# Kernel optimization log

Hardware: AMD Instinct MI355X
Metric: run time of the kernel (lower is better)

## Reference

```python
import jax, jax.numpy as jnp
import numpy as np

N, IN_CAPS, OUT_CH = 4096, 1152, 32
EPS = 1e-8

def squash(s, axis):
    # standard capsule squash: ||s||^2/(1+||s||^2) * s/||s||
    n2 = jnp.sum(s * s, axis=axis, keepdims=True)
    return (n2 / (1.0 + n2)) * s / jnp.sqrt(n2 + EPS)

def setup_inputs() -> dict:
    key = jax.random.key(0)
    k1, _ = jax.random.split(key)
    u_hat = jax.random.normal(k1, (N, IN_CAPS, OUT_CH), dtype=jnp.float32)
    # uniform routing prior: softmax of zeros over out_channels axis
    c = jnp.full((1, IN_CAPS, OUT_CH), 1.0 / OUT_CH, dtype=jnp.float32)
    return {"u_hat": u_hat, "c": c, "routings": 3}

def reference(u_hat, c, routings):
    out_channels = u_hat.shape[2]
    u = u_hat  # retain_grad=True: no stop_gradient on u
    for _ in range(routings - 1):
        v = squash(jnp.sum(u * c, axis=1), axis=1)          # (N, out_channels)
        b = u * v[:, None, :]                                # (N, in_caps, out_channels)
        c = jax.nn.softmax(b, axis=2)
    v = squash(jnp.sum(u_hat * c, axis=1), axis=1)
    return v[:, None, :] / 2.0 + 0.5                         # (N, 1, out_channels)
```

## Files before the change

kernel.cpp:

```cpp
#include <hip/hip_runtime.h>

#define IN_CAPS 1152
#define OUT_CH 32
#define PAD 33
#define BLOCK 576
#define NWAVES (BLOCK / 64)
#define ROWS_PER_THREAD (IN_CAPS / BLOCK)
#define F4_PER_THREAD (IN_CAPS * OUT_CH / 4 / BLOCK)
#define EPS 1e-8f

__global__ __launch_bounds__(BLOCK, 3)
void caps_route(const float* __restrict__ u_hat,
                const float* __restrict__ c0,
                const int* __restrict__ routings_p,
                float* __restrict__ out)
{
    __shared__ float u_s[IN_CAPS * PAD];
    __shared__ float swred[NWAVES * OUT_CH];
    __shared__ float vsh[OUT_CH];

    const int t = threadIdx.x;
    const int n = blockIdx.x;
    const int lane = t & 63;
    const int wave = t >> 6;

    const float4* __restrict__ u4 =
        reinterpret_cast<const float4*>(u_hat) + (size_t)n * (IN_CAPS * OUT_CH / 4);
    const float4* __restrict__ c4 = reinterpret_cast<const float4*>(c0);

    float p0 = 0.f, p1 = 0.f, p2 = 0.f, p3 = 0.f;
    #pragma unroll
    for (int k = 0; k < F4_PER_THREAD; ++k) {
        int f = t + k * BLOCK;
        float4 a = u4[f];
        float4 w = c4[f];
        int i  = f >> 3;
        int j0 = (f & 7) << 2;
        float* dst = &u_s[i * PAD + j0];
        dst[0] = a.x; dst[1] = a.y; dst[2] = a.z; dst[3] = a.w;
        p0 = fmaf(a.x, w.x, p0);
        p1 = fmaf(a.y, w.y, p1);
        p2 = fmaf(a.z, w.z, p2);
        p3 = fmaf(a.w, w.w, p3);
    }
    #pragma unroll
    for (int m = 8; m <= 32; m <<= 1) {
        p0 += __shfl_xor(p0, m);
        p1 += __shfl_xor(p1, m);
        p2 += __shfl_xor(p2, m);
        p3 += __shfl_xor(p3, m);
    }
    if (lane < 8) {
        swred[wave * OUT_CH + lane * 4 + 0] = p0;
        swred[wave * OUT_CH + lane * 4 + 1] = p1;
        swred[wave * OUT_CH + lane * 4 + 2] = p2;
        swred[wave * OUT_CH + lane * 4 + 3] = p3;
    }
    __syncthreads();
    if (t < OUT_CH) {
        float s = 0.f;
        #pragma unroll
        for (int w = 0; w < NWAVES; ++w) s += swred[w * OUT_CH + t];
        float n2 = s * s;
        #pragma unroll
        for (int m = 1; m <= 16; m <<= 1) n2 += __shfl_xor(n2, m);
        float scale = n2 / ((1.0f + n2) * sqrtf(n2 + EPS));
        vsh[t] = s * scale;
    }
    __syncthreads();

    const int iters = routings_p[0] - 1;
    for (int it = 0; it < iters; ++it) {
        float v[OUT_CH];
        #pragma unroll
        for (int j = 0; j < OUT_CH; ++j) v[j] = vsh[j];

        float acc[OUT_CH];
        #pragma unroll
        for (int j = 0; j < OUT_CH; ++j) acc[j] = 0.f;

        #pragma unroll
        for (int s = 0; s < ROWS_PER_THREAD; ++s) {
            const int i = t + s * BLOCK;
            const float* row = &u_s[i * PAD];
            float rr[OUT_CH], e[OUT_CH];
            float sum = 0.f;
            #pragma unroll
            for (int j = 0; j < OUT_CH; ++j) {
                rr[j] = row[j];
                e[j] = __expf(rr[j] * v[j]);
                sum += e[j];
            }
            float w = __builtin_amdgcn_rcpf(sum);
            #pragma unroll
            for (int j = 0; j < OUT_CH; ++j)
                acc[j] = fmaf(rr[j], e[j] * w, acc[j]);
        }

        #pragma unroll
        for (int j = 0; j < OUT_CH; ++j) {
            #pragma unroll
            for (int m = 1; m <= 32; m <<= 1)
                acc[j] += __shfl_xor(acc[j], m);
        }
        if (lane == 0) {
            #pragma unroll
            for (int j = 0; j < OUT_CH; ++j) swred[wave * OUT_CH + j] = acc[j];
        }
        __syncthreads();
        if (t < OUT_CH) {
            float s = 0.f;
            #pragma unroll
            for (int w = 0; w < NWAVES; ++w) s += swred[w * OUT_CH + t];
            float n2 = s * s;
            #pragma unroll
            for (int m = 1; m <= 16; m <<= 1) n2 += __shfl_xor(n2, m);
            float scale = n2 / ((1.0f + n2) * sqrtf(n2 + EPS));
            vsh[t] = s * scale;
        }
        __syncthreads();
    }

    if (t < OUT_CH) {
        out[(size_t)n * OUT_CH + t] = vsh[t] * 0.5f + 0.5f;
    }
}

extern "C" void kernel_launch(void* const* d_in, const int* in_sizes, int n_in,
                              void* d_out, int out_size, void* d_ws, size_t ws_size,
                              hipStream_t stream) {
    const float* u_hat   = (const float*)d_in[0];
    const float* c0      = (const float*)d_in[1];
    const int*   routing = (const int*)d_in[2];
    float* out = (float*)d_out;

    const int N = in_sizes[0] / (IN_CAPS * OUT_CH);
    caps_route<<<dim3(N), dim3(BLOCK), 0, stream>>>(u_hat, c0, routing, out);
}
```

Before: 971.6 us.

## Drop LDS staging of u_hat, re-read rows from global, use transpose-reduce

Removes the 147KB shared-memory copy of each sample's u_hat and instead re-reads rows from global memory (served by L2/MALL) in every routing iteration, with the block shrunk to 192 threads so more blocks fit per CU. The per-wave 32-channel shuffle reduction is replaced by a butterfly transpose-reduce that halves the live values at each stage, so the shuffle count drops from about 32x6 to about 32. The risk is extra global/L2 traffic, since each 147KB sample is read three times instead of once, in exchange for higher occupancy and no LDS capacity limit.

```diff
diff --git a/kernel.cpp b/kernel.cpp
--- a/kernel.cpp
+++ b/kernel.cpp
@@ -2,25 +2,23 @@
 
 #define IN_CAPS 1152
 #define OUT_CH 32
-#define PAD 33
-#define BLOCK 576
+#define BLOCK 192
 #define NWAVES (BLOCK / 64)
 #define ROWS_PER_THREAD (IN_CAPS / BLOCK)
 #define F4_PER_THREAD (IN_CAPS * OUT_CH / 4 / BLOCK)
 #define EPS 1e-8f
 
-__global__ __launch_bounds__(BLOCK, 3)
+__global__ __launch_bounds__(BLOCK, 4)
 void caps_route(const float* __restrict__ u_hat,
                 const float* __restrict__ c0,
                 const int* __restrict__ routings_p,
                 float* __restrict__ out)
 {
-    __shared__ float u_s[IN_CAPS * PAD];
     __shared__ float swred[NWAVES * OUT_CH];
     __shared__ float vsh[OUT_CH];
 
-    const int t = threadIdx.x;
-    const int n = blockIdx.x;
+    const int t    = threadIdx.x;
+    const int n    = blockIdx.x;
     const int lane = t & 63;
     const int wave = t >> 6;
 
@@ -31,13 +29,9 @@
     float p0 = 0.f, p1 = 0.f, p2 = 0.f, p3 = 0.f;
     #pragma unroll
     for (int k = 0; k < F4_PER_THREAD; ++k) {
-        int f = t + k * BLOCK;
-        float4 a = u4[f];
-        float4 w = c4[f];
-        int i  = f >> 3;
-        int j0 = (f & 7) << 2;
-        float* dst = &u_s[i * PAD + j0];
-        dst[0] = a.x; dst[1] = a.y; dst[2] = a.z; dst[3] = a.w;
+        const int f = t + k * BLOCK;
+        const float4 a = u4[f];
+        const float4 w = c4[f];
         p0 = fmaf(a.x, w.x, p0);
         p1 = fmaf(a.y, w.y, p1);
         p2 = fmaf(a.z, w.z, p2);
@@ -51,10 +45,8 @@
         p3 += __shfl_xor(p3, m);
     }
     if (lane < 8) {
-        swred[wave * OUT_CH + lane * 4 + 0] = p0;
-        swred[wave * OUT_CH + lane * 4 + 1] = p1;
-        swred[wave * OUT_CH + lane * 4 + 2] = p2;
-        swred[wave * OUT_CH + lane * 4 + 3] = p3;
+        float* dst = &swred[wave * OUT_CH + lane * 4];
+        dst[0] = p0; dst[1] = p1; dst[2] = p2; dst[3] = p3;
     }
     __syncthreads();
     if (t < OUT_CH) {
@@ -64,7 +56,7 @@
         float n2 = s * s;
         #pragma unroll
         for (int m = 1; m <= 16; m <<= 1) n2 += __shfl_xor(n2, m);
-        float scale = n2 / ((1.0f + n2) * sqrtf(n2 + EPS));
+        const float scale = n2 / ((1.0f + n2) * sqrtf(n2 + EPS));
         vsh[t] = s * scale;
     }
     __syncthreads();
@@ -82,31 +74,47 @@
         #pragma unroll
         for (int s = 0; s < ROWS_PER_THREAD; ++s) {
             const int i = t + s * BLOCK;
-            const float* row = &u_s[i * PAD];
-            float rr[OUT_CH], e[OUT_CH];
-            float sum = 0.f;
+            const float4* __restrict__ row = u4 + i * (OUT_CH / 4);
+            float rr[OUT_CH];
             #pragma unroll
-            for (int j = 0; j < OUT_CH; ++j) {
-                rr[j] = row[j];
-                e[j] = __expf(rr[j] * v[j]);
-                sum += e[j];
+            for (int k = 0; k < OUT_CH / 4; ++k) {
+                const float4 q = row[k];
+                rr[4*k+0] = q.x; rr[4*k+1] = q.y; rr[4*k+2] = q.z; rr[4*k+3] = q.w;
             }
-            float w = __builtin_amdgcn_rcpf(sum);
+            float s0 = 0.f, s1 = 0.f, s2 = 0.f, s3 = 0.f;
+            #pragma unroll
+            for (int j = 0; j < OUT_CH; j += 4) {
+                const float e0 = __expf(rr[j+0] * v[j+0]);
+                const float e1 = __expf(rr[j+1] * v[j+1]);
+                const float e2 = __expf(rr[j+2] * v[j+2]);
+                const float e3 = __expf(rr[j+3] * v[j+3]);
+                s0 += e0; s1 += e1; s2 += e2; s3 += e3;
+                rr[j+0] *= e0; rr[j+1] *= e1; rr[j+2] *= e2; rr[j+3] *= e3;
+            }
+            const float wr = __builtin_amdgcn_rcpf((s0 + s1) + (s2 + s3));
             #pragma unroll
             for (int j = 0; j < OUT_CH; ++j)
-                acc[j] = fmaf(rr[j], e[j] * w, acc[j]);
+                acc[j] = fmaf(rr[j], wr, acc[j]);
         }
 
         #pragma unroll
-        for (int j = 0; j < OUT_CH; ++j) {
+        for (int st = 0; st < 5; ++st) {
+            const int m    = 1 << st;
+            const int half = 16 >> st;
+            const bool up  = (lane & m) != 0;
             #pragma unroll
-            for (int m = 1; m <= 32; m <<= 1)
-                acc[j] += __shfl_xor(acc[j], m);
+            for (int j = 0; j < half; ++j) {
+                const float send = up ? acc[j] : acc[half + j];
+                const float keep = up ? acc[half + j] : acc[j];
+                acc[j] = keep + __shfl_xor(send, m);
+            }
         }
-        if (lane == 0) {
-            #pragma unroll
-            for (int j = 0; j < OUT_CH; ++j) swred[wave * OUT_CH + j] = acc[j];
-        }
+        acc[0] += __shfl_xor(acc[0], 32);
+
+        const int l5 = lane & 31;
+        const int ch = ((l5 & 1) << 4) | ((l5 & 2) << 2) | (l5 & 4)
+                     | ((l5 & 8) >> 2) | ((l5 & 16) >> 4);
+        if (lane < 32) swred[wave * OUT_CH + ch] = acc[0];
         __syncthreads();
         if (t < OUT_CH) {
             float s = 0.f;
@@ -115,15 +123,14 @@
             float n2 = s * s;
             #pragma unroll
             for (int m = 1; m <= 16; m <<= 1) n2 += __shfl_xor(n2, m);
-            float scale = n2 / ((1.0f + n2) * sqrtf(n2 + EPS));
+            const float scale = n2 / ((1.0f + n2) * sqrtf(n2 + EPS));
             vsh[t] = s * scale;
         }
         __syncthreads();
     }
 
-    if (t < OUT_CH) {
+    if (t < OUT_CH)
         out[(size_t)n * OUT_CH + t] = vsh[t] * 0.5f + 0.5f;
-    }
 }
 
 extern "C" void kernel_launch(void* const* d_in, const int* in_sizes, int n_in,
```

Result: slower. 1.682 ms (+73.1%).
